# Kernel tuning notes

Hardware: AMD Instinct MI355X
Metric: run time of the kernel (lower is better)

## Reference

```python
import jax, jax.numpy as jnp
import numpy as np

B, C, N = 16, 256, 2048
D = C // 8  # q/k channel dim = 32
EPS = 1e-5
NEG_SLOPE = 0.2


def _conv1x1(x, w, b):
    # x: [B,C,N], w: [O,C], b: [O] -> [B,O,N]
    return jnp.einsum('oc,bcn->bon', w, x) + b[None, :, None]


def _bn(y, gamma, beta):
    # BatchNorm1d training-mode: per-channel stats over (batch, length)
    m = y.mean(axis=(0, 2), keepdims=True)
    v = y.var(axis=(0, 2), keepdims=True)  # biased, matches torch normalization
    return (y - m) * jax.lax.rsqrt(v + EPS) * gamma[None, :, None] + beta[None, :, None]


def setup_inputs() -> dict:
    key = jax.random.key(0)
    ks = jax.random.split(key, 14)
    s_qk = 1.0 / np.sqrt(C)
    return {
        'x': jax.random.normal(ks[0], (B, C, N), dtype=jnp.float32),
        'q_w': jax.random.normal(ks[1], (D, C), dtype=jnp.float32) * s_qk,
        'q_b': jnp.zeros((D,), jnp.float32),
        'q_g': jnp.ones((D,), jnp.float32),
        'q_be': jnp.zeros((D,), jnp.float32),
        'k_w': jax.random.normal(ks[2], (D, C), dtype=jnp.float32) * s_qk,
        'k_b': jnp.zeros((D,), jnp.float32),
        'k_g': jnp.ones((D,), jnp.float32),
        'k_be': jnp.zeros((D,), jnp.float32),
        'v_w': jax.random.normal(ks[3], (C, C), dtype=jnp.float32) * s_qk,
        'v_b': jnp.zeros((C,), jnp.float32),
        'v_g': jnp.ones((C,), jnp.float32),
        'v_be': jnp.zeros((C,), jnp.float32),
    }


def reference(x, q_w, q_b, q_g, q_be, k_w, k_b, k_g, k_be, v_w, v_b, v_g, v_be):
    # q, k: conv1x1 -> BN (no activation); v: conv1x1 -> BN -> LeakyReLU(0.2)
    q = _bn(_conv1x1(x, q_w, q_b), q_g, q_be)          # [B,D,N]
    k = _bn(_conv1x1(x, k_w, k_b), k_g, k_be)          # [B,D,N]
    v = jax.nn.leaky_relu(_bn(_conv1x1(x, v_w, v_b), v_g, v_be), NEG_SLOPE)  # [B,C,N]
    energy = jnp.einsum('bdn,bdm->bnm', q, k)          # [B,N,N]
    attn = jax.nn.softmax(energy, axis=-1)
    o = jnp.einsum('bcm,bnm->bcn', v, attn)            # attn applied over points
    return o + x
```

## Files before the change

### kernel.cpp

```cpp
#include <hip/hip_runtime.h>

#define BATCH 16
#define CH    256
#define NPT   2048
#define DQK   32
#define OTOT  320
#define EPSB  1e-5f
#define SLOPE 0.2f

typedef __attribute__((ext_vector_type(8))) short bf16x8;
typedef __attribute__((ext_vector_type(4))) float f32x4;

__device__ __forceinline__ unsigned short f2bf(float f) {
    unsigned u = __float_as_uint(f);
    u = (u + 0x7FFFu + ((u >> 16) & 1u)) >> 16;
    return (unsigned short)u;
}
__device__ __forceinline__ float bf2f(unsigned short h) {
    return __uint_as_float(((unsigned)h) << 16);
}

__global__ __launch_bounds__(256) void prep_kernel(
    const float* __restrict__ qw, const float* __restrict__ qb,
    const float* __restrict__ kw, const float* __restrict__ kb,
    const float* __restrict__ vw, const float* __restrict__ vb,
    unsigned short* __restrict__ Whi, unsigned short* __restrict__ Wlo,
    float* __restrict__ Bv)
{
    int idx = blockIdx.x * 256 + threadIdx.x;
    int o = idx >> 8, c = idx & 255;
    float w;
    if (o < 32)      w = qw[(size_t)o * CH + c];
    else if (o < 64) w = kw[(size_t)(o - 32) * CH + c];
    else             w = vw[(size_t)(o - 64) * CH + c];
    unsigned short wh = f2bf(w);
    float rem = w - bf2f(wh);
    Whi[idx] = wh;
    Wlo[idx] = f2bf(rem);
    if (idx < OTOT) {
        int oo = idx;
        float bb;
        if (oo < 32)      bb = qb[oo];
        else if (oo < 64) bb = kb[oo - 32];
        else              bb = vb[oo - 64];
        Bv[oo] = bb;
    }
}

__global__ __launch_bounds__(256) void conv_kernel(
    const float* __restrict__ x,
    const unsigned short* __restrict__ Whi, const unsigned short* __restrict__ Wlo,
    const float* __restrict__ Bv,
    unsigned short* __restrict__ Ybf,
    float* __restrict__ Sum, float* __restrict__ Sq)
{
    int ob = blockIdx.x * 64;
    int n0 = blockIdx.y * 128;
    int b  = blockIdx.z;
    int tid = threadIdx.x;
    int w = tid >> 6, lane = tid & 63;
    int quad = lane >> 4, l16 = lane & 15;
    int wo = w >> 1, wn = w & 1;

    __shared__ unsigned short Xh[128][40];
    __shared__ unsigned short Xl[128][40];

    int nl = tid & 127;
    int ch = tid >> 7;
    const float* xb = x + (size_t)b * CH * NPT + n0 + nl;

    f32x4 acc[2][4];
#pragma unroll
    for (int ot = 0; ot < 2; ++ot)
#pragma unroll
        for (int nt = 0; nt < 4; ++nt)
            acc[ot][nt] = (f32x4){0.f, 0.f, 0.f, 0.f};

    float xv[16];
#pragma unroll
    for (int i = 0; i < 16; ++i)
        xv[i] = xb[(size_t)(ch * 16 + i) * NPT];

    for (int ks = 0; ks < 8; ++ks) {
        __syncthreads();
#pragma unroll
        for (int g = 0; g < 4; ++g) {
            ushort4 h4, l4;
            unsigned short* ph = (unsigned short*)&h4;
            unsigned short* pl = (unsigned short*)&l4;
#pragma unroll
            for (int j = 0; j < 4; ++j) {
                float f = xv[g * 4 + j];
                unsigned short h = f2bf(f);
                ph[j] = h;
                pl[j] = f2bf(f - bf2f(h));
            }
            *(ushort4*)&Xh[nl][ch * 16 + g * 4] = h4;
            *(ushort4*)&Xl[nl][ch * 16 + g * 4] = l4;
        }
        __syncthreads();

        if (ks < 7) {
#pragma unroll
            for (int i = 0; i < 16; ++i)
                xv[i] = xb[(size_t)((ks + 1) * 32 + ch * 16 + i) * NPT];
        }

        bf16x8 ah[2], al[2];
#pragma unroll
        for (int ot = 0; ot < 2; ++ot) {
            size_t orow = (size_t)(ob + wo * 32 + ot * 16 + l16) * 256 + ks * 32 + quad * 8;
            ah[ot] = *(const bf16x8*)(Whi + orow);
            al[ot] = *(const bf16x8*)(Wlo + orow);
        }
#pragma unroll
        for (int nt = 0; nt < 4; ++nt) {
            int nr = wn * 64 + nt * 16 + l16;
            bf16x8 bh = *(const bf16x8*)&Xh[nr][quad * 8];
            bf16x8 bl = *(const bf16x8*)&Xl[nr][quad * 8];
#pragma unroll
            for (int ot = 0; ot < 2; ++ot) {
                acc[ot][nt] = __builtin_amdgcn_mfma_f32_16x16x32_bf16(ah[ot], bh, acc[ot][nt], 0, 0, 0);
                acc[ot][nt] = __builtin_amdgcn_mfma_f32_16x16x32_bf16(ah[ot], bl, acc[ot][nt], 0, 0, 0);
                acc[ot][nt] = __builtin_amdgcn_mfma_f32_16x16x32_bf16(al[ot], bh, acc[ot][nt], 0, 0, 0);
            }
        }
    }

#pragma unroll
    for (int ot = 0; ot < 2; ++ot) {
        int obase = ob + wo * 32 + ot * 16 + quad * 4;
        float bias[4], sv[4], sq[4];
#pragma unroll
        for (int r = 0; r < 4; ++r) {
            bias[r] = Bv[obase + r];
            sv[r] = 0.f; sq[r] = 0.f;
        }
#pragma unroll
        for (int nt = 0; nt < 4; ++nt) {
            int n = n0 + wn * 64 + nt * 16 + l16;
#pragma unroll
            for (int r = 0; r < 4; ++r) {
                float v = acc[ot][nt][r] + bias[r];
                Ybf[((size_t)b * OTOT + obase + r) * NPT + n] = f2bf(v);
                sv[r] += v; sq[r] += v * v;
            }
        }
#pragma unroll
        for (int r = 0; r < 4; ++r) {
            float a = sv[r], q = sq[r];
            a += __shfl_xor(a, 1); q += __shfl_xor(q, 1);
            a += __shfl_xor(a, 2); q += __shfl_xor(q, 2);
            a += __shfl_xor(a, 4); q += __shfl_xor(q, 4);
            a += __shfl_xor(a, 8); q += __shfl_xor(q, 8);
            if (l16 == 0) {
                atomicAdd(&Sum[obase + r], a);
                atomicAdd(&Sq[obase + r], q);
            }
        }
    }
}

__global__ __launch_bounds__(320) void finalize_kernel(
    const float* __restrict__ Sum, const float* __restrict__ Sq,
    const float* __restrict__ qg, const float* __restrict__ qbe,
    const float* __restrict__ kg, const float* __restrict__ kbe,
    const float* __restrict__ vg, const float* __restrict__ vbe,
    float* __restrict__ A, float* __restrict__ Cc)
{
    int o = threadIdx.x;
    if (o >= OTOT) return;
    const float inv = 1.0f / (BATCH * NPT);
    float mean = Sum[o] * inv;
    float var  = Sq[o] * inv - mean * mean;
    float g, be;
    if (o < 32)      { g = qg[o];      be = qbe[o];      }
    else if (o < 64) { g = kg[o - 32]; be = kbe[o - 32]; }
    else             { g = vg[o - 64]; be = vbe[o - 64]; }
    float a = g * rsqrtf(var + EPSB);
    A[o]  = a;
    Cc[o] = be - mean * a;
}

__global__ __launch_bounds__(256) void pack_kernel(
    const unsigned short* __restrict__ Ybf,
    const float* __restrict__ A, const float* __restrict__ Cc,
    unsigned short* __restrict__ QKt, unsigned short* __restrict__ Vbf)
{
    int b = blockIdx.y, n0 = blockIdx.x * 64;
    int tid = threadIdx.x;

    for (int e = tid; e < 4096; e += 256) {
        int c = e >> 4, n4 = (e & 15) * 4;
        ushort4 v4 = *(const ushort4*)(Ybf + ((size_t)b * OTOT + 64 + c) * NPT + n0 + n4);
        float a = A[64 + c], cc = Cc[64 + c];
        ushort4 w4;
        unsigned short* pi = (unsigned short*)&v4;
        unsigned short* po = (unsigned short*)&w4;
#pragma unroll
        for (int i = 0; i < 4; ++i) {
            float y = bf2f(pi[i]) * a + cc;
            y = (y > 0.f) ? y : SLOPE * y;
            po[i] = f2bf(y);
        }
        *(ushort4*)(Vbf + ((size_t)b * CH + c) * NPT + n0 + n4) = w4;
    }

    __shared__ unsigned short T[64][72];
    for (int e = tid; e < 1024; e += 256) {
        int o = e >> 4, n4 = (e & 15) * 4;
        ushort4 v4 = *(const ushort4*)(Ybf + ((size_t)b * OTOT + o) * NPT + n0 + n4);
        float a = A[o], cc = Cc[o];
        unsigned short* pi = (unsigned short*)&v4;
#pragma unroll
        for (int i = 0; i < 4; ++i)
            T[n4 + i][o] = f2bf(bf2f(pi[i]) * a + cc);
    }
    __syncthreads();
    for (int e = tid; e < 1024; e += 256) {
        int nn = e >> 4, o4 = (e & 15) * 4;
        ushort4 v4 = *(const ushort4*)&T[nn][o4];
        *(ushort4*)(QKt + ((size_t)b * NPT + n0 + nn) * 64 + o4) = v4;
    }
}

__global__ __launch_bounds__(256, 4) void attn_kernel(
    const unsigned short* __restrict__ QKt,
    const unsigned short* __restrict__ Vbf,
    const float* __restrict__ x,
    float* __restrict__ out)
{
    int L = blockIdx.x;
    int xcd = L & 7, k = L >> 3;
    int gi = k >> 5, n0i = k & 31;
    int grp = xcd * 4 + gi;
    int b = grp >> 1, z = grp & 1;
    int n0 = n0i * 64;

    int tid = threadIdx.x;
    int w = tid >> 6, lane = tid & 63;
    int quad = lane >> 4, l16 = lane & 15;

    const unsigned short* QK = QKt + (size_t)b * NPT * 64;
    const unsigned short* V  = Vbf + ((size_t)b * CH + z * 128) * NPT;

    __shared__ unsigned short Pbf[64][72];
    __shared__ float rsw[4][64];
    __shared__ float rtot[64];

    bf16x8 qa[4];
#pragma unroll
    for (int nt = 0; nt < 4; ++nt)
        qa[nt] = *(const bf16x8*)(QK + ((size_t)(n0 + nt * 16 + l16)) * 64 + quad * 8);

    f32x4 acc[4][2];
#pragma unroll
    for (int nt = 0; nt < 4; ++nt)
#pragma unroll
        for (int ct = 0; ct < 2; ++ct)
            acc[nt][ct] = (f32x4){0.f, 0.f, 0.f, 0.f};

    float rsum[4][4];
#pragma unroll
    for (int nt = 0; nt < 4; ++nt)
#pragma unroll
        for (int r = 0; r < 4; ++r) rsum[nt][r] = 0.f;

    const f32x4 zero4 = (f32x4){0.f, 0.f, 0.f, 0.f};

    for (int mt = 0; mt < NPT / 64; ++mt) {
        bf16x8 kb = *(const bf16x8*)(QK + ((size_t)(mt * 64 + w * 16 + l16)) * 64 + 32 + quad * 8);

        __syncthreads();

#pragma unroll
        for (int nt = 0; nt < 4; ++nt) {
            f32x4 s = __builtin_amdgcn_mfma_f32_16x16x32_bf16(qa[nt], kb, zero4, 0, 0, 0);
#pragma unroll
            for (int r = 0; r < 4; ++r) {
                float p = __expf(s[r]);
                rsum[nt][r] += p;
                Pbf[nt * 16 + quad * 4 + r][w * 16 + l16] = f2bf(p);
            }
        }
        __syncthreads();

#pragma unroll
        for (int ks = 0; ks < 2; ++ks) {
            bf16x8 pa[4];
#pragma unroll
            for (int nt = 0; nt < 4; ++nt)
                pa[nt] = *(const bf16x8*)&Pbf[nt * 16 + l16][ks * 32 + quad * 8];
#pragma unroll
            for (int ct = 0; ct < 2; ++ct) {
                const unsigned short* vp =
                    V + ((size_t)(w * 32 + ct * 16 + l16)) * NPT + mt * 64 + ks * 32 + quad * 8;
                bf16x8 vb = *(const bf16x8*)vp;
#pragma unroll
                for (int nt = 0; nt < 4; ++nt)
                    acc[nt][ct] = __builtin_amdgcn_mfma_f32_16x16x32_bf16(pa[nt], vb, acc[nt][ct], 0, 0, 0);
            }
        }
    }

#pragma unroll
    for (int nt = 0; nt < 4; ++nt)
#pragma unroll
        for (int r = 0; r < 4; ++r) {
            float v = rsum[nt][r];
            v += __shfl_xor(v, 1);
            v += __shfl_xor(v, 2);
            v += __shfl_xor(v, 4);
            v += __shfl_xor(v, 8);
            if (l16 == 0) rsw[w][nt * 16 + quad * 4 + r] = v;
        }
    __syncthreads();
    if (tid < 64)
        rtot[tid] = 1.0f / (rsw[0][tid] + rsw[1][tid] + rsw[2][tid] + rsw[3][tid]);
    __syncthreads();

    float rin[4][4];
#pragma unroll
    for (int nt = 0; nt < 4; ++nt)
#pragma unroll
        for (int r = 0; r < 4; ++r) rin[nt][r] = rtot[nt * 16 + quad * 4 + r];

#pragma unroll
    for (int nt = 0; nt < 4; ++nt)
#pragma unroll
        for (int ct = 0; ct < 2; ++ct) {
            int c = z * 128 + w * 32 + ct * 16 + l16;
            int n = n0 + nt * 16 + quad * 4;
            size_t gi4 = ((size_t)b * CH + c) * NPT + n;
            float4 xv = *(const float4*)(x + gi4);
            float4 o;
            o.x = acc[nt][ct][0] * rin[nt][0] + xv.x;
            o.y = acc[nt][ct][1] * rin[nt][1] + xv.y;
            o.z = acc[nt][ct][2] * rin[nt][2] + xv.z;
            o.w = acc[nt][ct][3] * rin[nt][3] + xv.w;
            *(float4*)(out + gi4) = o;
        }
}

extern "C" void kernel_launch(void* const* d_in, const int* in_sizes, int n_in,
                              void* d_out, int out_size, void* d_ws, size_t ws_size,
                              hipStream_t stream)
{
    const float* x   = (const float*)d_in[0];
    const float* qw  = (const float*)d_in[1];
    const float* qb  = (const float*)d_in[2];
    const float* qg  = (const float*)d_in[3];
    const float* qbe = (const float*)d_in[4];
    const float* kw  = (const float*)d_in[5];
    const float* kb  = (const float*)d_in[6];
    const float* kg  = (const float*)d_in[7];
    const float* kbe = (const float*)d_in[8];
    const float* vw  = (const float*)d_in[9];
    const float* vb  = (const float*)d_in[10];
    const float* vg  = (const float*)d_in[11];
    const float* vbe = (const float*)d_in[12];
    float* out = (float*)d_out;

    unsigned short* Ybf = (unsigned short*)d_ws;
    unsigned short* QKt = Ybf + (size_t)BATCH * OTOT * NPT;
    unsigned short* Vbf = QKt + (size_t)BATCH * NPT * 64;
    float* tail = (float*)(Vbf + (size_t)BATCH * CH * NPT);
    float* Sum = tail;
    float* Sq  = tail + OTOT;
    float* A   = tail + 2 * OTOT;
    float* Cc  = tail + 3 * OTOT;
    unsigned short* Whi = QKt;
    unsigned short* Wlo = Whi + (size_t)CH * OTOT;
    float* Bv = (float*)(Wlo + (size_t)CH * OTOT);

    hipMemsetAsync(Sum, 0, 2 * OTOT * sizeof(float), stream);
    prep_kernel    <<<320, 256, 0, stream>>>(qw, qb, kw, kb, vw, vb, Whi, Wlo, Bv);
    conv_kernel    <<<dim3(5, 16, 16), 256, 0, stream>>>(x, Whi, Wlo, Bv, Ybf, Sum, Sq);
    finalize_kernel<<<1, 320, 0, stream>>>(Sum, Sq, qg, qbe, kg, kbe, vg, vbe, A, Cc);
    pack_kernel    <<<dim3(NPT / 64, BATCH), 256, 0, stream>>>(Ybf, A, Cc, QKt, Vbf);
    attn_kernel    <<<1024, 256, 0, stream>>>(QKt, Vbf, x, out);
}
```

Before: 276.2 us.

## Keep softmax probabilities in registers via lane shuffles instead of shared memory

The attention kernel is restructured so each wave owns 16 query rows and all 128 channels of its half. It computes S^T with MFMA, exponentiates, and repacks the probabilities into B-operand layout using cross-lane shuffles instead of a shared-memory tile. This removes both block barriers and LDS traffic per key tile, and the row-sum reduction no longer needs shared memory. The cost is that every wave now loads all V rows from global memory (4x V traffic per block), and the output stores become scalar strided writes instead of float4.

```diff
diff --git a/kernel.cpp b/kernel.cpp
--- a/kernel.cpp
+++ b/kernel.cpp
@@ -18,6 +18,9 @@
 }
 __device__ __forceinline__ float bf2f(unsigned short h) {
     return __uint_as_float(((unsigned)h) << 16);
+}
+__device__ __forceinline__ unsigned pack2(float a, float b) {
+    return (unsigned)f2bf(a) | ((unsigned)f2bf(b) << 16);
 }
 
 __global__ __launch_bounds__(256) void prep_kernel(
@@ -244,102 +247,65 @@
     const unsigned short* QK = QKt + (size_t)b * NPT * 64;
     const unsigned short* V  = Vbf + ((size_t)b * CH + z * 128) * NPT;
 
-    __shared__ unsigned short Pbf[64][72];
-    __shared__ float rsw[4][64];
-    __shared__ float rtot[64];
-
-    bf16x8 qa[4];
-#pragma unroll
-    for (int nt = 0; nt < 4; ++nt)
-        qa[nt] = *(const bf16x8*)(QK + ((size_t)(n0 + nt * 16 + l16)) * 64 + quad * 8);
-
-    f32x4 acc[4][2];
-#pragma unroll
-    for (int nt = 0; nt < 4; ++nt)
-#pragma unroll
-        for (int ct = 0; ct < 2; ++ct)
-            acc[nt][ct] = (f32x4){0.f, 0.f, 0.f, 0.f};
-
-    float rsum[4][4];
-#pragma unroll
-    for (int nt = 0; nt < 4; ++nt)
-#pragma unroll
-        for (int r = 0; r < 4; ++r) rsum[nt][r] = 0.f;
+    bf16x8 qf = *(const bf16x8*)(QK + ((size_t)(n0 + w * 16 + l16)) * 64 + quad * 8);
+
+    f32x4 o[8];
+#pragma unroll
+    for (int ct = 0; ct < 8; ++ct) o[ct] = (f32x4){0.f, 0.f, 0.f, 0.f};
+    float rsum = 0.f;
 
     const f32x4 zero4 = (f32x4){0.f, 0.f, 0.f, 0.f};
-
-    for (int mt = 0; mt < NPT / 64; ++mt) {
-        bf16x8 kb = *(const bf16x8*)(QK + ((size_t)(mt * 64 + w * 16 + l16)) * 64 + 32 + quad * 8);
-
-        __syncthreads();
-
-#pragma unroll
-        for (int nt = 0; nt < 4; ++nt) {
-            f32x4 s = __builtin_amdgcn_mfma_f32_16x16x32_bf16(qa[nt], kb, zero4, 0, 0, 0);
-#pragma unroll
-            for (int r = 0; r < 4; ++r) {
-                float p = __expf(s[r]);
-                rsum[nt][r] += p;
-                Pbf[nt * 16 + quad * 4 + r][w * 16 + l16] = f2bf(p);
-            }
-        }
-        __syncthreads();
-
-#pragma unroll
-        for (int ks = 0; ks < 2; ++ks) {
-            bf16x8 pa[4];
-#pragma unroll
-            for (int nt = 0; nt < 4; ++nt)
-                pa[nt] = *(const bf16x8*)&Pbf[nt * 16 + l16][ks * 32 + quad * 8];
-#pragma unroll
-            for (int ct = 0; ct < 2; ++ct) {
-                const unsigned short* vp =
-                    V + ((size_t)(w * 32 + ct * 16 + l16)) * NPT + mt * 64 + ks * 32 + quad * 8;
-                bf16x8 vb = *(const bf16x8*)vp;
-#pragma unroll
-                for (int nt = 0; nt < 4; ++nt)
-                    acc[nt][ct] = __builtin_amdgcn_mfma_f32_16x16x32_bf16(pa[nt], vb, acc[nt][ct], 0, 0, 0);
-            }
-        }
-    }
-
-#pragma unroll
-    for (int nt = 0; nt < 4; ++nt)
+    const int sA = ((quad & 1) * 2) * 16 + l16;
+    const int sB = sA + 16;
+    const bool hiTile = quad >= 2;
+
+    for (int m0 = 0; m0 < NPT; m0 += 32) {
+        bf16x8 kf0 = *(const bf16x8*)(QK + ((size_t)(m0 + l16)) * 64 + 32 + quad * 8);
+        bf16x8 kf1 = *(const bf16x8*)(QK + ((size_t)(m0 + 16 + l16)) * 64 + 32 + quad * 8);
+
+        f32x4 st0 = __builtin_amdgcn_mfma_f32_16x16x32_bf16(kf0, qf, zero4, 0, 0, 0);
+        f32x4 st1 = __builtin_amdgcn_mfma_f32_16x16x32_bf16(kf1, qf, zero4, 0, 0, 0);
+
+        float p0 = __expf(st0[0]), p1 = __expf(st0[1]);
+        float p2 = __expf(st0[2]), p3 = __expf(st0[3]);
+        float q0 = __expf(st1[0]), q1 = __expf(st1[1]);
+        float q2 = __expf(st1[2]), q3 = __expf(st1[3]);
+        rsum += (p0 + p1) + (p2 + p3) + (q0 + q1) + (q2 + q3);
+
+        unsigned t0pk0 = pack2(p0, p1), t0pk1 = pack2(p2, p3);
+        unsigned t1pk0 = pack2(q0, q1), t1pk1 = pack2(q2, q3);
+
+        unsigned a0 = __shfl(t0pk0, sA), b0 = __shfl(t1pk0, sA);
+        unsigned a1 = __shfl(t0pk1, sA), b1 = __shfl(t1pk1, sA);
+        unsigned a2 = __shfl(t0pk0, sB), b2 = __shfl(t1pk0, sB);
+        unsigned a3 = __shfl(t0pk1, sB), b3 = __shfl(t1pk1, sB);
+        union { unsigned u[4]; bf16x8 v; } pf;
+        pf.u[0] = hiTile ? b0 : a0;
+        pf.u[1] = hiTile ? b1 : a1;
+        pf.u[2] = hiTile ? b2 : a2;
+        pf.u[3] = hiTile ? b3 : a3;
+
+#pragma unroll
+        for (int ct = 0; ct < 8; ++ct) {
+            bf16x8 vf = *(const bf16x8*)(V + ((size_t)(ct * 16 + l16)) * NPT + m0 + quad * 8);
+            o[ct] = __builtin_amdgcn_mfma_f32_16x16x32_bf16(vf, pf.v, o[ct], 0, 0, 0);
+        }
+    }
+
+    rsum += __shfl_xor(rsum, 16);
+    rsum += __shfl_xor(rsum, 32);
+    float rtot = 1.0f / rsum;
+
+    int n = n0 + w * 16 + l16;
+#pragma unroll
+    for (int ct = 0; ct < 8; ++ct) {
+        int cbase = z * 128 + ct * 16 + quad * 4;
 #pragma unroll
         for (int r = 0; r < 4; ++r) {
-            float v = rsum[nt][r];
-            v += __shfl_xor(v, 1);
-            v += __shfl_xor(v, 2);
-            v += __shfl_xor(v, 4);
-            v += __shfl_xor(v, 8);
-            if (l16 == 0) rsw[w][nt * 16 + quad * 4 + r] = v;
-        }
-    __syncthreads();
-    if (tid < 64)
-        rtot[tid] = 1.0f / (rsw[0][tid] + rsw[1][tid] + rsw[2][tid] + rsw[3][tid]);
-    __syncthreads();
-
-    float rin[4][4];
-#pragma unroll
-    for (int nt = 0; nt < 4; ++nt)
-#pragma unroll
-        for (int r = 0; r < 4; ++r) rin[nt][r] = rtot[nt * 16 + quad * 4 + r];
-
-#pragma unroll
-    for (int nt = 0; nt < 4; ++nt)
-#pragma unroll
-        for (int ct = 0; ct < 2; ++ct) {
-            int c = z * 128 + w * 32 + ct * 16 + l16;
-            int n = n0 + nt * 16 + quad * 4;
-            size_t gi4 = ((size_t)b * CH + c) * NPT + n;
-            float4 xv = *(const float4*)(x + gi4);
-            float4 o;
-            o.x = acc[nt][ct][0] * rin[nt][0] + xv.x;
-            o.y = acc[nt][ct][1] * rin[nt][1] + xv.y;
-            o.z = acc[nt][ct][2] * rin[nt][2] + xv.z;
-            o.w = acc[nt][ct][3] * rin[nt][3] + xv.w;
-            *(float4*)(out + gi4) = o;
-        }
+            size_t gidx = ((size_t)b * CH + cbase + r) * NPT + n;
+            out[gidx] = o[ct][r] * rtot + x[gidx];
+        }
+    }
 }
 
 extern "C" void kernel_launch(void* const* d_in, const int* in_sizes, int n_in,
```

Measured after the change: 475.5 us. 1.72x slower.
